# Optimization experiments

Hardware: AMD Instinct MI355X
Metric: run time of the kernel (lower is better)

Reference implementation:

```python
import jax, jax.numpy as jnp
import numpy as np

L_LIST = [0, 1, 2, 3]
PAIRS = [(l1, l2) for l1 in L_LIST for l2 in L_LIST if l1 <= l2]
S, I, N = 8, 32, 8  # structures, atoms per structure, radial functions


def setup_inputs() -> dict:
    key = jax.random.key(0)
    inp = {}
    for l in L_LIST:
        key, k1, k2 = jax.random.split(key, 3)
        inp[f"c_in_l{l}"] = jax.random.normal(k1, (S, I, 2 * l + 1, N), dtype=jnp.float32)
        inp[f"c_tgt_l{l}"] = jax.random.normal(k2, (S, I, 2 * l + 1, N), dtype=jnp.float32)
    for (l1, l2) in PAIRS:
        key, k1 = jax.random.split(key)
        # overlap block stored pre-permuted: [S, i1, m1, n1, i2, m2, n2]
        inp[f"ovlp_l{l1}_l{l2}"] = jax.random.normal(
            k1, (S, I, 2 * l1 + 1, N, I, 2 * l2 + 1, N), dtype=jnp.float32)
    return inp


def _rho_loss(c_in, c_tgt, ovlp):
    # delta_coeffs = input - target, per (l) block (single species)
    d = {l: c_in[l] - c_tgt[l] for l in L_LIST}
    total = jnp.float32(0.0)
    for (l1, l2) in PAIRS:
        O = ovlp[(l1, l2)]
        # tensordot(c1, O, dims=3) over (i1, m1, n1), batched over structures s
        t = jnp.einsum('simn,simnjpq->sjpq', d[l1], O)
        # tensordot(t, c2, dims=3) over (i2, m2, n2), then sum over structures
        b = jnp.einsum('sjpq,sjpq->', t, d[l2])
        # diagonal blocks (l1==l2, a1==a2) counted once, off-diagonal twice
        total = total + (b if l1 == l2 else 2.0 * b)
    return total


def reference(c_in_l0, c_tgt_l0, c_in_l1, c_tgt_l1, c_in_l2, c_tgt_l2,
              c_in_l3, c_tgt_l3, ovlp_l0_l0, ovlp_l0_l1, ovlp_l0_l2,
              ovlp_l0_l3, ovlp_l1_l1, ovlp_l1_l2, ovlp_l1_l3, ovlp_l2_l2,
              ovlp_l2_l3, ovlp_l3_l3):
    c_in = {0: c_in_l0, 1: c_in_l1, 2: c_in_l2, 3: c_in_l3}
    c_tgt = {0: c_tgt_l0, 1: c_tgt_l1, 2: c_tgt_l2, 3: c_tgt_l3}
    ovlp = {(0, 0): ovlp_l0_l0, (0, 1): ovlp_l0_l1, (0, 2): ovlp_l0_l2,
            (0, 3): ovlp_l0_l3, (1, 1): ovlp_l1_l1, (1, 2): ovlp_l1_l2,
            (1, 3): ovlp_l1_l3, (2, 2): ovlp_l2_l2, (2, 3): ovlp_l2_l3,
            (3, 3): ovlp_l3_l3}
    return _rho_loss(c_in, c_tgt, ovlp)
```

## Files before the change

kernel.cpp:

```cpp
#include <hip/hip_runtime.h>


#define NUM_S 8

template <int K1, int K2, int W>
__device__ __forceinline__ float pair_sum(const float* __restrict__ O,
                                          const float* __restrict__ ci1,
                                          const float* __restrict__ ct1,
                                          const float* __restrict__ ci2,
                                          const float* __restrict__ ct2,
                                          int tid, int nthreads) {
    constexpr int C2    = K2 / 4;
    constexpr int PER_S = K1 * C2;
    constexpr int TOT4  = NUM_S * PER_S;

    const float4* __restrict__ O4 = (const float4*)O;
    float acc = 0.0f;
    for (int idx = tid; idx < TOT4; idx += nthreads) {
        const int s   = idx / PER_S;
        const int rem = idx - s * PER_S;
        const int r1  = rem / C2;
        const int c2  = rem - r1 * C2;

        const float4 o = O4[idx];

        const float d1 = ci1[s * K1 + r1] - ct1[s * K1 + r1];

        const float4 a = ((const float4*)(ci2 + s * K2))[c2];
        const float4 b = ((const float4*)(ct2 + s * K2))[c2];

        float dot;
        dot = o.x * (a.x - b.x);
        dot = fmaf(o.y, (a.y - b.y), dot);
        dot = fmaf(o.z, (a.z - b.z), dot);
        dot = fmaf(o.w, (a.w - b.w), dot);

        acc = fmaf(d1, dot, acc);
    }
    return (float)W * acc;
}

__global__ __launch_bounds__(256) void rho_loss_kernel(
    const float* __restrict__ ci0, const float* __restrict__ ct0,
    const float* __restrict__ ci1, const float* __restrict__ ct1,
    const float* __restrict__ ci2, const float* __restrict__ ct2,
    const float* __restrict__ ci3, const float* __restrict__ ct3,
    const float* __restrict__ O00, const float* __restrict__ O01,
    const float* __restrict__ O02, const float* __restrict__ O03,
    const float* __restrict__ O11, const float* __restrict__ O12,
    const float* __restrict__ O13, const float* __restrict__ O22,
    const float* __restrict__ O23, const float* __restrict__ O33,
    float* __restrict__ out) {
    const int tid      = blockIdx.x * blockDim.x + threadIdx.x;
    const int nthreads = gridDim.x * blockDim.x;

    float acc = 0.0f;
    acc += pair_sum< 256,  256, 1>(O00, ci0, ct0, ci0, ct0, tid, nthreads);
    acc += pair_sum< 256,  768, 2>(O01, ci0, ct0, ci1, ct1, tid, nthreads);
    acc += pair_sum< 256, 1280, 2>(O02, ci0, ct0, ci2, ct2, tid, nthreads);
    acc += pair_sum< 256, 1792, 2>(O03, ci0, ct0, ci3, ct3, tid, nthreads);
    acc += pair_sum< 768,  768, 1>(O11, ci1, ct1, ci1, ct1, tid, nthreads);
    acc += pair_sum< 768, 1280, 2>(O12, ci1, ct1, ci2, ct2, tid, nthreads);
    acc += pair_sum< 768, 1792, 2>(O13, ci1, ct1, ci3, ct3, tid, nthreads);
    acc += pair_sum<1280, 1280, 1>(O22, ci2, ct2, ci2, ct2, tid, nthreads);
    acc += pair_sum<1280, 1792, 2>(O23, ci2, ct2, ci3, ct3, tid, nthreads);
    acc += pair_sum<1792, 1792, 1>(O33, ci3, ct3, ci3, ct3, tid, nthreads);

    for (int off = 32; off > 0; off >>= 1)
        acc += __shfl_down(acc, off, 64);

    __shared__ float wsum[4];
    const int lane = threadIdx.x & 63;
    const int wid  = threadIdx.x >> 6;
    if (lane == 0) wsum[wid] = acc;
    __syncthreads();
    if (threadIdx.x == 0) {
        float s = wsum[0] + wsum[1] + wsum[2] + wsum[3];
        atomicAdd(out, s);
    }
}

extern "C" void kernel_launch(void* const* d_in, const int* in_sizes, int n_in,
                              void* d_out, int out_size, void* d_ws, size_t ws_size,
                              hipStream_t stream) {
    (void)in_sizes; (void)n_in; (void)d_ws; (void)ws_size; (void)out_size;

    const float* ci0 = (const float*)d_in[0];
    const float* ct0 = (const float*)d_in[1];
    const float* ci1 = (const float*)d_in[2];
    const float* ct1 = (const float*)d_in[3];
    const float* ci2 = (const float*)d_in[4];
    const float* ct2 = (const float*)d_in[5];
    const float* ci3 = (const float*)d_in[6];
    const float* ct3 = (const float*)d_in[7];
    const float* O00 = (const float*)d_in[8];
    const float* O01 = (const float*)d_in[9];
    const float* O02 = (const float*)d_in[10];
    const float* O03 = (const float*)d_in[11];
    const float* O11 = (const float*)d_in[12];
    const float* O12 = (const float*)d_in[13];
    const float* O13 = (const float*)d_in[14];
    const float* O22 = (const float*)d_in[15];
    const float* O23 = (const float*)d_in[16];
    const float* O33 = (const float*)d_in[17];

    hipMemsetAsync(d_out, 0, sizeof(float), stream);

    const int threads = 256;
    const int blocks  = 2048;
    rho_loss_kernel<<<blocks, threads, 0, stream>>>(
        ci0, ct0, ci1, ct1, ci2, ct2, ci3, ct3,
        O00, O01, O02, O03, O11, O12, O13, O22, O23, O33,
        (float*)d_out);
}
```

Measured before the change: 349.7 us.

## Precompute coefficient deltas and assign overlap rows to wavefronts

A small pre-kernel computes all input-minus-target deltas once into a global buffer. The main kernel then gives each wavefront whole rows of each overlap block, with multiple float4 loads per lane issued up front and the row's delta loaded once per row instead of per element. This removes redundant subtraction and division-based index math and adds memory-level parallelism. Per-pair rotation offsets spread tail rows across wavefronts. The cost is one extra kernel launch and a global scratch buffer.

Result: no change. 344.5 us (-1.5%).

```diff
diff --git a/kernel.cpp b/kernel.cpp
--- a/kernel.cpp
+++ b/kernel.cpp
@@ -3,76 +3,96 @@
 
 #define NUM_S 8
 
-template <int K1, int K2, int W>
-__device__ __forceinline__ float pair_sum(const float* __restrict__ O,
-                                          const float* __restrict__ ci1,
-                                          const float* __restrict__ ct1,
-                                          const float* __restrict__ ci2,
-                                          const float* __restrict__ ct2,
-                                          int tid, int nthreads) {
-    constexpr int C2    = K2 / 4;
-    constexpr int PER_S = K1 * C2;
-    constexpr int TOT4  = NUM_S * PER_S;
+__device__ float g_d[32768];
 
-    const float4* __restrict__ O4 = (const float4*)O;
-    float acc = 0.0f;
-    for (int idx = tid; idx < TOT4; idx += nthreads) {
-        const int s   = idx / PER_S;
-        const int rem = idx - s * PER_S;
-        const int r1  = rem / C2;
-        const int c2  = rem - r1 * C2;
+__global__ __launch_bounds__(256) void compute_d_kernel(
+    const float* __restrict__ ci0, const float* __restrict__ ct0,
+    const float* __restrict__ ci1, const float* __restrict__ ct1,
+    const float* __restrict__ ci2, const float* __restrict__ ct2,
+    const float* __restrict__ ci3, const float* __restrict__ ct3) {
+    const int t = blockIdx.x * 256 + threadIdx.x;
+    float v;
+    if (t < 2048)       v = ci0[t]         - ct0[t];
+    else if (t < 8192)  v = ci1[t - 2048]  - ct1[t - 2048];
+    else if (t < 18432) v = ci2[t - 8192]  - ct2[t - 8192];
+    else                v = ci3[t - 18432] - ct3[t - 18432];
+    g_d[t] = v;
+}
 
-        const float4 o = O4[idx];
+#define NWAVES 8192
 
-        const float d1 = ci1[s * K1 + r1] - ct1[s * K1 + r1];
+template <int K1, int K2, int W, int ROT>
+__device__ __forceinline__ float pair_sum_rows(const float4* __restrict__ O4,
+                                               const float* __restrict__ d1,
+                                               const float* __restrict__ d2,
+                                               int wid, int lane) {
+    constexpr int C2q    = K2 / 4;
+    constexpr int ROUNDS = C2q / 64;
+    constexpr int NROWS  = NUM_S * K1;
 
-        const float4 a = ((const float4*)(ci2 + s * K2))[c2];
-        const float4 b = ((const float4*)(ct2 + s * K2))[c2];
+    float ax = 0.f, ay = 0.f, az = 0.f, aw = 0.f;
+    for (int t = (wid + ROT) & (NWAVES - 1); t < NROWS; t += NWAVES) {
+        const int s = t / K1;
+        const float4* __restrict__ o = O4 + (size_t)t * C2q + lane;
+        const float4* __restrict__ v = (const float4*)(d2 + s * K2) + lane;
 
-        float dot;
-        dot = o.x * (a.x - b.x);
-        dot = fmaf(o.y, (a.y - b.y), dot);
-        dot = fmaf(o.z, (a.z - b.z), dot);
-        dot = fmaf(o.w, (a.w - b.w), dot);
+        float4 ov[ROUNDS], vv[ROUNDS];
+#pragma unroll
+        for (int j = 0; j < ROUNDS; ++j) ov[j] = o[j * 64];
+#pragma unroll
+        for (int j = 0; j < ROUNDS; ++j) vv[j] = v[j * 64];
 
-        acc = fmaf(d1, dot, acc);
+        const float dd = d1[t];
+
+        float dx = 0.f, dy = 0.f, dz = 0.f, dw = 0.f;
+#pragma unroll
+        for (int j = 0; j < ROUNDS; ++j) {
+            dx = fmaf(ov[j].x, vv[j].x, dx);
+            dy = fmaf(ov[j].y, vv[j].y, dy);
+            dz = fmaf(ov[j].z, vv[j].z, dz);
+            dw = fmaf(ov[j].w, vv[j].w, dw);
+        }
+        ax = fmaf(dd, dx, ax);
+        ay = fmaf(dd, dy, ay);
+        az = fmaf(dd, dz, az);
+        aw = fmaf(dd, dw, aw);
     }
-    return (float)W * acc;
+    return (float)W * ((ax + ay) + (az + aw));
 }
 
 __global__ __launch_bounds__(256) void rho_loss_kernel(
-    const float* __restrict__ ci0, const float* __restrict__ ct0,
-    const float* __restrict__ ci1, const float* __restrict__ ct1,
-    const float* __restrict__ ci2, const float* __restrict__ ct2,
-    const float* __restrict__ ci3, const float* __restrict__ ct3,
     const float* __restrict__ O00, const float* __restrict__ O01,
     const float* __restrict__ O02, const float* __restrict__ O03,
     const float* __restrict__ O11, const float* __restrict__ O12,
     const float* __restrict__ O13, const float* __restrict__ O22,
     const float* __restrict__ O23, const float* __restrict__ O33,
     float* __restrict__ out) {
-    const int tid      = blockIdx.x * blockDim.x + threadIdx.x;
-    const int nthreads = gridDim.x * blockDim.x;
+    const int lane = threadIdx.x & 63;
+    const int wid  = blockIdx.x * 4 + (threadIdx.x >> 6);
 
-    float acc = 0.0f;
-    acc += pair_sum< 256,  256, 1>(O00, ci0, ct0, ci0, ct0, tid, nthreads);
-    acc += pair_sum< 256,  768, 2>(O01, ci0, ct0, ci1, ct1, tid, nthreads);
-    acc += pair_sum< 256, 1280, 2>(O02, ci0, ct0, ci2, ct2, tid, nthreads);
-    acc += pair_sum< 256, 1792, 2>(O03, ci0, ct0, ci3, ct3, tid, nthreads);
-    acc += pair_sum< 768,  768, 1>(O11, ci1, ct1, ci1, ct1, tid, nthreads);
-    acc += pair_sum< 768, 1280, 2>(O12, ci1, ct1, ci2, ct2, tid, nthreads);
-    acc += pair_sum< 768, 1792, 2>(O13, ci1, ct1, ci3, ct3, tid, nthreads);
-    acc += pair_sum<1280, 1280, 1>(O22, ci2, ct2, ci2, ct2, tid, nthreads);
-    acc += pair_sum<1280, 1792, 2>(O23, ci2, ct2, ci3, ct3, tid, nthreads);
-    acc += pair_sum<1792, 1792, 1>(O33, ci3, ct3, ci3, ct3, tid, nthreads);
+    const float* D0 = g_d;
+    const float* D1 = g_d + 2048;
+    const float* D2 = g_d + 8192;
+    const float* D3 = g_d + 18432;
+
+    float acc = 0.f;
+    acc += pair_sum_rows< 256,  256, 1,    0>((const float4*)O00, D0, D0, wid, lane);
+    acc += pair_sum_rows< 256,  768, 2,  819>((const float4*)O01, D0, D1, wid, lane);
+    acc += pair_sum_rows< 256, 1280, 2, 1638>((const float4*)O02, D0, D2, wid, lane);
+    acc += pair_sum_rows< 256, 1792, 2, 2457>((const float4*)O03, D0, D3, wid, lane);
+    acc += pair_sum_rows< 768,  768, 1, 3276>((const float4*)O11, D1, D1, wid, lane);
+    acc += pair_sum_rows< 768, 1280, 2, 4095>((const float4*)O12, D1, D2, wid, lane);
+    acc += pair_sum_rows< 768, 1792, 2, 4914>((const float4*)O13, D1, D3, wid, lane);
+    acc += pair_sum_rows<1280, 1280, 1, 5733>((const float4*)O22, D2, D2, wid, lane);
+    acc += pair_sum_rows<1280, 1792, 2, 6552>((const float4*)O23, D2, D3, wid, lane);
+    acc += pair_sum_rows<1792, 1792, 1, 7371>((const float4*)O33, D3, D3, wid, lane);
 
     for (int off = 32; off > 0; off >>= 1)
         acc += __shfl_down(acc, off, 64);
 
     __shared__ float wsum[4];
-    const int lane = threadIdx.x & 63;
-    const int wid  = threadIdx.x >> 6;
-    if (lane == 0) wsum[wid] = acc;
+    const int lwid = threadIdx.x >> 6;
+    if (lane == 0) wsum[lwid] = acc;
     __syncthreads();
     if (threadIdx.x == 0) {
         float s = wsum[0] + wsum[1] + wsum[2] + wsum[3];
@@ -106,10 +126,9 @@
 
     hipMemsetAsync(d_out, 0, sizeof(float), stream);
 
-    const int threads = 256;
-    const int blocks  = 2048;
-    rho_loss_kernel<<<blocks, threads, 0, stream>>>(
-        ci0, ct0, ci1, ct1, ci2, ct2, ci3, ct3,
-        O00, O01, O02, O03, O11, O12, O13, O22, O23, O33,
-        (float*)d_out);
+    compute_d_kernel<<<128, 256, 0, stream>>>(ci0, ct0, ci1, ct1,
+                                              ci2, ct2, ci3, ct3);
+
+    rho_loss_kernel<<<2048, 256, 0, stream>>>(
+        O00, O01, O02, O03, O11, O12, O13, O22, O23, O33, (float*)d_out);
 }
```
